# Kernel tuning notes

Hardware: AMD Instinct MI355X
Metric: run time of the kernel (lower is better)

The kernel has to match this reference:

```python
import jax, jax.numpy as jnp
import numpy as np

DIM = 384
K = 10
LN_EPS = 1e-5


def sqdist(src, dst):
    # src [B,N,3], dst [B,M,3] -> [B,N,M] squared euclidean
    d = -2.0 * jnp.einsum('bnc,bmc->bnm', src, dst)
    d += jnp.sum(src ** 2, -1)[:, :, None]
    d += jnp.sum(dst ** 2, -1)[:, None, :]
    return d


def index_points(points, idx):
    # points [B,M,C], idx [B,...] int -> [B,...,C]
    B = points.shape[0]
    flat = idx.reshape(B, -1)
    out = jnp.take_along_axis(points, flat[..., None], axis=1)
    return out.reshape(idx.shape + (points.shape[-1],))


def setup_inputs() -> dict:
    key = jax.random.key(0)
    ks = jax.random.split(key, 10)
    B, N, C = 4, 2048, DIM
    inp = {
        'q': jax.random.normal(ks[0], (B, N, C), jnp.float32),
        'q_pos': jax.random.normal(ks[1], (B, N, 3), jnp.float32),
        # proj_v_off: Linear(dim, dim)
        'Wv': jax.random.normal(ks[2], (C, C), jnp.float32) * 0.02,
        'bv': jnp.zeros((C,), jnp.float32),
        # linear_offset: Linear(2*dim, dim) -> LayerNorm(dim) -> GELU -> Linear(dim, 3, bias=False)
        'W1': jax.random.normal(ks[3], (2 * C, C), jnp.float32) * 0.02,
        'b1': jnp.zeros((C,), jnp.float32),
        'ln_g': jnp.ones((C,), jnp.float32),
        'ln_b': jnp.zeros((C,), jnp.float32),
        'W2': jax.random.normal(ks[4], (C, 3), jnp.float32) * 0.02,
        # knn_map: Linear(2*dim, dim) -> LeakyReLU(0.2)
        'Wk': jax.random.normal(ks[5], (2 * C, C), jnp.float32) * 0.02,
        'bk': jnp.zeros((C,), jnp.float32),
    }
    return inp


def reference(q, q_pos, Wv, bv, W1, b1, ln_g, ln_b, W2, Wk, bk):
    B, N, C = q.shape
    # knn_point: k nearest v_pos for each q_pos (self-attn: v=q, v_pos=q_pos)
    neg_d, idx = jax.lax.top_k(-sqdist(q_pos, q_pos), K)          # idx [B,N,K]

    v_off = q @ Wv + bv                                           # [B,N,C]
    off_local_v = index_points(v_off, idx)                        # [B,N,K,C]
    qk = jnp.broadcast_to(q[:, :, None, :], (B, N, K, C))
    shift_feat = jnp.concatenate([off_local_v, qk], axis=-1)      # [B,N,K,2C]

    h = shift_feat @ W1 + b1
    mu = jnp.mean(h, -1, keepdims=True)
    var = jnp.mean((h - mu) ** 2, -1, keepdims=True)
    h = (h - mu) * jax.lax.rsqrt(var + LN_EPS) * ln_g + ln_b
    h = jax.nn.gelu(h, approximate=False)
    offset = jnp.tanh(h @ W2)                                     # [B,N,K,3]

    local_v_pos = index_points(q_pos, idx)                        # [B,N,K,3]
    scale = (jnp.max(local_v_pos, -2) - jnp.min(local_v_pos, -2))[:, :, None, :] * 0.5
    shift_pos = (local_v_pos + offset * scale).reshape(B, N * K, 3)

    # three_nn: 3 nearest v_pos per shifted point (squared dists, as pointnet2 CUDA)
    neg_d3, idx3 = jax.lax.top_k(-sqdist(shift_pos, q_pos), 3)    # [B,N*K,3]
    dist = -neg_d3
    recip = 1.0 / (dist + 1e-8)
    weight = recip / jnp.sum(recip, -1, keepdims=True)

    nb = index_points(q, idx3)                                    # [B,N*K,3,C]
    interp = jnp.sum(nb * weight[..., None], axis=-2)             # [B,N*K,C]
    interp = interp.reshape(B, N, K, C)

    feature = jnp.concatenate([interp - qk, qk], axis=-1)         # [B,N,K,2C]
    out = jax.nn.leaky_relu(feature @ Wk + bk, 0.2)               # [B,N,K,C]
    return jnp.max(out, axis=-2)                                  # [B,N,C]
```

## Files before the change

### kernel.cpp

```cpp
#include <hip/hip_runtime.h>
#include <hip/hip_bf16.h>
#include <math.h>

#define C_DIM 384
#define N_PTS 2048
#define K_NN 10
#define NK (N_PTS * K_NN)
#define LN_EPS_F 1e-5f

#define TCC 8
#define TCHUNK (N_PTS / TCC)

typedef __attribute__((ext_vector_type(8))) short short8v;
typedef __attribute__((ext_vector_type(4))) float f32x4;

__device__ __forceinline__ float wave_sum64(float v) {
#pragma unroll
  for (int off = 32; off > 0; off >>= 1) v += __shfl_xor(v, off, 64);
  return v;
}

__device__ __forceinline__ unsigned long long shfl_xor_u64(unsigned long long v, int m) {
  return (unsigned long long)__shfl_xor((long long)v, m, 64);
}

__device__ __forceinline__ unsigned short f32_to_bf16_rne(float x) {
  unsigned int u = __float_as_uint(x);
  u += 0x7FFFu + ((u >> 16) & 1u);
  return (unsigned short)(u >> 16);
}

__global__ __launch_bounds__(256) void conv_q_kernel(
    const float* __restrict__ q, unsigned short* __restrict__ outp) {
  const size_t i = ((size_t)blockIdx.x * 256 + threadIdx.x) * 4;
  float4 v = *reinterpret_cast<const float4*>(&q[i]);
  ushort4 o;
  o.x = f32_to_bf16_rne(v.x); o.y = f32_to_bf16_rne(v.y);
  o.z = f32_to_bf16_rne(v.z); o.w = f32_to_bf16_rne(v.w);
  *reinterpret_cast<ushort4*>(&outp[i]) = o;
}

__global__ __launch_bounds__(256) void conv_wkT_kernel(
    const float* __restrict__ Wk, unsigned short* __restrict__ Bt) {
  __shared__ unsigned short tile[64][68];
  const int k0 = blockIdx.x * 64;
  const int sn = blockIdx.y;
  const int s  = sn / 6;
  const int n0 = (sn % 6) * 64;
  const int t = threadIdx.x;
  const int r = t >> 2;
  const int cc = t & 3;
#pragma unroll
  for (int h = 0; h < 4; ++h) {
    const int c = cc * 16 + h * 4;
    float4 v = *reinterpret_cast<const float4*>(
        &Wk[(size_t)(s * 384 + k0 + r) * C_DIM + n0 + c]);
    tile[c + 0][r] = f32_to_bf16_rne(v.x);
    tile[c + 1][r] = f32_to_bf16_rne(v.y);
    tile[c + 2][r] = f32_to_bf16_rne(v.z);
    tile[c + 3][r] = f32_to_bf16_rne(v.w);
  }
  __syncthreads();
#pragma unroll
  for (int h = 0; h < 4; ++h) {
    const int col = cc * 16 + h * 4;
    ushort4 o;
    o.x = tile[r][col + 0]; o.y = tile[r][col + 1];
    o.z = tile[r][col + 2]; o.w = tile[r][col + 3];
    *reinterpret_cast<ushort4*>(
        &Bt[(size_t)(s * 384 + n0 + r) * C_DIM + k0 + col]) = o;
  }
}

__global__ __launch_bounds__(64) void mfma_qaqb_kernel(
    const unsigned short* __restrict__ qbf, const unsigned short* __restrict__ Bt,
    const float* __restrict__ bk, float* __restrict__ qa, float* __restrict__ qb) {
  const int lane = threadIdx.x;
  const int bx = blockIdx.x;
  const int seg = bx / 6;
  const int n0 = (bx % 6) * 64;
  const int m0 = blockIdx.y * 64;
  const unsigned short* Bs = Bt + (size_t)seg * C_DIM * C_DIM;
  const int lm = lane & 15;
  const int lk = (lane >> 4) * 8;
  f32x4 acc[4][4] = {};
#pragma unroll 2
  for (int k0 = 0; k0 < C_DIM; k0 += 32) {
    short8v a[4], b[4];
#pragma unroll
    for (int i = 0; i < 4; ++i)
      a[i] = *reinterpret_cast<const short8v*>(
          &qbf[(size_t)(m0 + i * 16 + lm) * C_DIM + k0 + lk]);
#pragma unroll
    for (int j = 0; j < 4; ++j)
      b[j] = *reinterpret_cast<const short8v*>(
          &Bs[(size_t)(n0 + j * 16 + lm) * C_DIM + k0 + lk]);
#pragma unroll
    for (int i = 0; i < 4; ++i)
#pragma unroll
      for (int j = 0; j < 4; ++j)
        acc[i][j] = __builtin_amdgcn_mfma_f32_16x16x32_bf16(a[i], b[j], acc[i][j], 0, 0, 0);
  }
  const int rb = (lane >> 4) * 4;
#pragma unroll
  for (int i = 0; i < 4; ++i)
#pragma unroll
    for (int j = 0; j < 4; ++j) {
      const int c = n0 + j * 16 + lm;
#pragma unroll
      for (int r = 0; r < 4; ++r) {
        const int m = m0 + i * 16 + rb + r;
        float v = acc[i][j][r];
        if (seg == 0) qa[(size_t)m * C_DIM + c] = v;
        else          qb[(size_t)m * C_DIM + c] = v + bk[c];
      }
    }
}

__global__ __launch_bounds__(256) void sgemm_q2_kernel(
    const float* __restrict__ q,
    const float* __restrict__ B0, const float* __restrict__ B1,
    const float* __restrict__ bias0, const float* __restrict__ bias1,
    float* __restrict__ O0, float* __restrict__ O1) {
  __shared__ float As[32][68];
  __shared__ float Bs[32][132];
  const int bx = blockIdx.x;
  const int seg = bx / 3;
  const int n0 = (bx % 3) * 128;
  const int m0 = blockIdx.y * 64;
  const float* Bp = seg ? B1 : B0;
  const float* bp = seg ? bias1 : bias0;
  float* Op = seg ? O1 : O0;
  const int tid = threadIdx.x;
  const int tn = tid & 15;
  const int tm = tid >> 4;
  float acc[4][8] = {};
  for (int k0 = 0; k0 < C_DIM; k0 += 32) {
#pragma unroll
    for (int h = 0; h < 2; ++h) {
      const int idx = tid + h * 256;
      const int r = idx >> 3;
      const int kc = (idx & 7) * 4;
      float4 a4 = *reinterpret_cast<const float4*>(
          &q[(size_t)(m0 + r) * C_DIM + k0 + kc]);
      As[kc + 0][r] = a4.x; As[kc + 1][r] = a4.y;
      As[kc + 2][r] = a4.z; As[kc + 3][r] = a4.w;
    }
#pragma unroll
    for (int h = 0; h < 4; ++h) {
      const int idx = tid + h * 256;
      const int br = idx >> 5;
      const int bc = (idx & 31) * 4;
      float4 b4 = *reinterpret_cast<const float4*>(
          &Bp[(size_t)(k0 + br) * C_DIM + n0 + bc]);
      *reinterpret_cast<float4*>(&Bs[br][bc]) = b4;
    }
    __syncthreads();
#pragma unroll
    for (int kk = 0; kk < 32; ++kk) {
      float4 a4 = *reinterpret_cast<const float4*>(&As[kk][tm << 2]);
      float4 b0 = *reinterpret_cast<const float4*>(&Bs[kk][tn << 2]);
      float4 b1 = *reinterpret_cast<const float4*>(&Bs[kk][(tn << 2) + 64]);
      float av[4] = {a4.x, a4.y, a4.z, a4.w};
      float bw[8] = {b0.x, b0.y, b0.z, b0.w, b1.x, b1.y, b1.z, b1.w};
#pragma unroll
      for (int i = 0; i < 4; ++i)
#pragma unroll
        for (int j = 0; j < 8; ++j) acc[i][j] = fmaf(av[i], bw[j], acc[i][j]);
    }
    __syncthreads();
  }
#pragma unroll
  for (int i = 0; i < 4; ++i) {
    const int m = m0 + (tm << 2) + i;
    const int c0 = n0 + (tn << 2);
    float4 o0, o1;
    o0.x = acc[i][0]; o0.y = acc[i][1]; o0.z = acc[i][2]; o0.w = acc[i][3];
    o1.x = acc[i][4]; o1.y = acc[i][5]; o1.z = acc[i][6]; o1.w = acc[i][7];
    if (bp) {
      o0.x += bp[c0 + 0]; o0.y += bp[c0 + 1]; o0.z += bp[c0 + 2]; o0.w += bp[c0 + 3];
      o1.x += bp[c0 + 64]; o1.y += bp[c0 + 65]; o1.z += bp[c0 + 66]; o1.w += bp[c0 + 67];
    }
    *reinterpret_cast<float4*>(&Op[(size_t)m * C_DIM + c0]) = o0;
    *reinterpret_cast<float4*>(&Op[(size_t)m * C_DIM + c0 + 64]) = o1;
  }
}

__global__ __launch_bounds__(256) void gemm384_kernel(
    const float* __restrict__ A, const float* __restrict__ W,
    const float* __restrict__ bias, float* __restrict__ Out) {
  __shared__ float As[32][64];
  __shared__ float Bs[32][64];
  const int bm = blockIdx.y * 64;
  const int bn = blockIdx.x * 64;
  const int tid = threadIdx.x;
  const int tx = tid & 15;
  const int ty = tid >> 4;
  const int arow = tid >> 3;
  const int akc  = (tid & 7) << 2;
  const int brow = tid >> 4;
  const int bnc  = (tid & 15) << 2;
  float acc[4][4] = {{0.f, 0.f, 0.f, 0.f}, {0.f, 0.f, 0.f, 0.f},
                     {0.f, 0.f, 0.f, 0.f}, {0.f, 0.f, 0.f, 0.f}};
  for (int k0 = 0; k0 < C_DIM; k0 += 32) {
#pragma unroll
    for (int h = 0; h < 2; ++h) {
      float4 a4 = *reinterpret_cast<const float4*>(
          &A[(size_t)(bm + arow + h * 32) * C_DIM + k0 + akc]);
      As[akc + 0][arow + h * 32] = a4.x;
      As[akc + 1][arow + h * 32] = a4.y;
      As[akc + 2][arow + h * 32] = a4.z;
      As[akc + 3][arow + h * 32] = a4.w;
      float4 b4 = *reinterpret_cast<const float4*>(
          &W[(size_t)(k0 + brow + h * 16) * C_DIM + bn + bnc]);
      *reinterpret_cast<float4*>(&Bs[brow + h * 16][bnc]) = b4;
    }
    __syncthreads();
#pragma unroll
    for (int k = 0; k < 32; ++k) {
      float4 a4 = *reinterpret_cast<const float4*>(&As[k][ty << 2]);
      float4 b4 = *reinterpret_cast<const float4*>(&Bs[k][tx << 2]);
      float av[4] = {a4.x, a4.y, a4.z, a4.w};
      float bw[4] = {b4.x, b4.y, b4.z, b4.w};
#pragma unroll
      for (int i = 0; i < 4; ++i)
#pragma unroll
        for (int j = 0; j < 4; ++j) acc[i][j] = fmaf(av[i], bw[j], acc[i][j]);
    }
    __syncthreads();
  }
#pragma unroll
  for (int i = 0; i < 4; ++i) {
    const int m = bm + (ty << 2) + i;
    const int n0 = bn + (tx << 2);
    float4 o;
    o.x = acc[i][0]; o.y = acc[i][1]; o.z = acc[i][2]; o.w = acc[i][3];
    if (bias) {
      o.x += bias[n0 + 0]; o.y += bias[n0 + 1];
      o.z += bias[n0 + 2]; o.w += bias[n0 + 3];
    }
    *reinterpret_cast<float4*>(&Out[(size_t)m * C_DIM + n0]) = o;
  }
}

__global__ __launch_bounds__(256) void knn_wave_kernel(
    const float* __restrict__ q_pos, int* __restrict__ idx_out,
    float* __restrict__ scale_out) {
  const int wid = threadIdx.x >> 6;
  const int lane = threadIdx.x & 63;
  const int q = blockIdx.x * 4 + wid;
  const int b = q >> 11;
  const int qi = q & 2047;
  __shared__ float4 sc[N_PTS];
  const float* P = q_pos + (size_t)b * N_PTS * 3;
  for (int i = threadIdx.x; i < N_PTS; i += 256) {
    float x = P[i * 3 + 0], y = P[i * 3 + 1], z = P[i * 3 + 2];
    float s = __fadd_rn(__fadd_rn(__fmul_rn(x, x), __fmul_rn(y, y)), __fmul_rn(z, z));
    sc[i] = make_float4(x, y, z, s);
  }
  __syncthreads();
  const float4 qc = sc[qi];
  unsigned long long bd[K_NN];
#pragma unroll
  for (int t = 0; t < K_NN; ++t) bd[t] = ~0ull;
  for (int t = 0; t < N_PTS / 64; ++t) {
    const int j = (t << 6) + lane;
    float4 c = sc[j];
    float dot = __fadd_rn(__fadd_rn(__fmul_rn(qc.x, c.x), __fmul_rn(qc.y, c.y)),
                          __fmul_rn(qc.z, c.z));
    float d = __fadd_rn(__fadd_rn(__fmul_rn(-2.f, dot), qc.w), c.w);
    unsigned int db = __float_as_uint(d);
    db ^= (unsigned int)((int)db >> 31) | 0x80000000u;
    unsigned long long v = ((unsigned long long)db << 32) | (unsigned int)j;
    if (v < bd[K_NN - 1]) {
#pragma unroll
      for (int r = 0; r < K_NN; ++r) {
        bool lt = bd[r] < v;
        unsigned long long lo = lt ? bd[r] : v;
        unsigned long long hi = lt ? v : bd[r];
        bd[r] = lo; v = hi;
      }
    }
  }
  unsigned long long cur = bd[0];
  unsigned long long mine = 0;
#pragma unroll
  for (int r = 0; r < K_NN; ++r) {
    unsigned long long m = cur;
#pragma unroll
    for (int off = 32; off >= 1; off >>= 1) {
      unsigned long long o = shfl_xor_u64(m, off);
      m = (o < m) ? o : m;
    }
    if (cur == m) {
      cur = bd[1];
#pragma unroll
      for (int s = 1; s < K_NN - 1; ++s) bd[s] = bd[s + 1];
      bd[K_NN - 1] = ~0ull;
    }
    if (lane == r) mine = m;
  }
  const int nidx = (int)(mine & 0xFFFFFFFFull);
  if (lane < K_NN) idx_out[(size_t)q * K_NN + lane] = nidx;
  float mnx, mny, mnz, mxx, mxy, mxz;
  if (lane < K_NN) {
    float4 c = sc[nidx];
    mnx = c.x; mny = c.y; mnz = c.z; mxx = c.x; mxy = c.y; mxz = c.z;
  } else {
    mnx = 1e30f; mny = 1e30f; mnz = 1e30f;
    mxx = -1e30f; mxy = -1e30f; mxz = -1e30f;
  }
#pragma unroll
  for (int off = 32; off >= 1; off >>= 1) {
    mnx = fminf(mnx, __shfl_xor(mnx, off, 64));
    mny = fminf(mny, __shfl_xor(mny, off, 64));
    mnz = fminf(mnz, __shfl_xor(mnz, off, 64));
    mxx = fmaxf(mxx, __shfl_xor(mxx, off, 64));
    mxy = fmaxf(mxy, __shfl_xor(mxy, off, 64));
    mxz = fmaxf(mxz, __shfl_xor(mxz, off, 64));
  }
  if (lane == 0) {
    scale_out[(size_t)q * 3 + 0] = (mxx - mnx) * 0.5f;
    scale_out[(size_t)q * 3 + 1] = (mxy - mny) * 0.5f;
    scale_out[(size_t)q * 3 + 2] = (mxz - mnz) * 0.5f;
  }
}

__global__ __launch_bounds__(256) void mid_kernel(
    const float* __restrict__ hv, const float* __restrict__ hq,
    const int* __restrict__ idx, const float* __restrict__ scale,
    const float* __restrict__ q_pos, const float* __restrict__ ln_g,
    const float* __restrict__ ln_b, const float* __restrict__ W2,
    float* __restrict__ shift_pos) {
  const int wid = threadIdx.x >> 6;
  const int lane = threadIdx.x & 63;
  const long row = (long)blockIdx.x * 4 + wid;
  const long bn = row / K_NN;
  const int b = (int)(bn / N_PTS);
  const int g = idx[row];
  const float* hvp = hv + ((size_t)b * N_PTS + g) * C_DIM;
  const float* hqp = hq + (size_t)bn * C_DIM;
  float h[6];
  float s = 0.f;
#pragma unroll
  for (int r = 0; r < 6; ++r) {
    h[r] = hvp[lane + (r << 6)] + hqp[lane + (r << 6)];
    s += h[r];
  }
  s = wave_sum64(s);
  const float mu = s / 384.f;
  float hc[6];
  float vs = 0.f;
#pragma unroll
  for (int r = 0; r < 6; ++r) { hc[r] = h[r] - mu; vs += hc[r] * hc[r]; }
  vs = wave_sum64(vs);
  const float inv = 1.f / sqrtf(vs / 384.f + LN_EPS_F);
  float o0 = 0.f, o1 = 0.f, o2 = 0.f;
#pragma unroll
  for (int r = 0; r < 6; ++r) {
    const int c = lane + (r << 6);
    float y = hc[r] * inv * ln_g[c] + ln_b[c];
    float ge = 0.5f * y * (1.f + erff(y * 0.70710678118654752f));
    o0 += ge * W2[c * 3 + 0];
    o1 += ge * W2[c * 3 + 1];
    o2 += ge * W2[c * 3 + 2];
  }
  o0 = wave_sum64(o0); o1 = wave_sum64(o1); o2 = wave_sum64(o2);
  if (lane < 3) {
    float o = (lane == 0) ? o0 : ((lane == 1) ? o1 : o2);
    float off = tanhf(o);
    float lv = q_pos[((size_t)b * N_PTS + g) * 3 + lane];
    float sc = scale[(size_t)bn * 3 + lane];
    shift_pos[(size_t)row * 3 + lane] = lv + off * sc;
  }
}

__global__ __launch_bounds__(256) void three_nn_part_kernel(
    const float* __restrict__ shift_pos, const float* __restrict__ q_pos,
    float* __restrict__ pd3, int* __restrict__ pi3) {
  const int cc = blockIdx.x;
  const int qc = blockIdx.y;
  const int b = qc / (NK / 256);
  const float* P = q_pos + (size_t)b * N_PTS * 3;
  __shared__ float4 sc[TCHUNK];
  const int c0 = cc * TCHUNK;
  for (int i = threadIdx.x; i < TCHUNK; i += 256) {
    float x = P[(c0 + i) * 3 + 0], y = P[(c0 + i) * 3 + 1], z = P[(c0 + i) * 3 + 2];
    float s = __fadd_rn(__fadd_rn(__fmul_rn(x, x), __fmul_rn(y, y)), __fmul_rn(z, z));
    sc[i] = make_float4(x, y, z, s);
  }
  __syncthreads();
  const long jq = (long)qc * 256 + threadIdx.x;
  const float* S = shift_pos + (size_t)jq * 3;
  const float px = S[0], py = S[1], pz = S[2];
  const float ps = __fadd_rn(__fadd_rn(__fmul_rn(px, px), __fmul_rn(py, py)),
                             __fmul_rn(pz, pz));
  float d0 = 1e30f, d1 = 1e30f, d2 = 1e30f;
  int i0 = 0, i1 = 0, i2 = 0;
  for (int j = 0; j < TCHUNK; ++j) {
    float4 c = sc[j];
    float dot = __fadd_rn(__fadd_rn(__fmul_rn(px, c.x), __fmul_rn(py, c.y)),
                          __fmul_rn(pz, c.z));
    float d = __fadd_rn(__fadd_rn(__fmul_rn(-2.f, dot), ps), c.w);
    if (d < d2) {
      int j0 = c0 + j;
      if (d < d0)      { d2 = d1; i2 = i1; d1 = d0; i1 = i0; d0 = d; i0 = j0; }
      else if (d < d1) { d2 = d1; i2 = i1; d1 = d; i1 = j0; }
      else             { d2 = d; i2 = j0; }
    }
  }
  const size_t base = ((size_t)jq * TCC + cc) * 3;
  pd3[base + 0] = d0; pd3[base + 1] = d1; pd3[base + 2] = d2;
  pi3[base + 0] = i0; pi3[base + 1] = i1; pi3[base + 2] = i2;
}

__global__ __launch_bounds__(256) void three_nn_merge_kernel(
    const float* __restrict__ pd3, const int* __restrict__ pi3,
    int* __restrict__ idx3, float* __restrict__ w3) {
  const long jq = (long)blockIdx.x * 256 + threadIdx.x;
  float d0 = 1e30f, d1 = 1e30f, d2 = 1e30f;
  int i0 = 0, i1 = 0, i2 = 0;
  const size_t base = (size_t)jq * TCC * 3;
  for (int e = 0; e < TCC * 3; ++e) {
    float d = pd3[base + e];
    if (d < d2) {
      int j0 = pi3[base + e];
      if (d < d0)      { d2 = d1; i2 = i1; d1 = d0; i1 = i0; d0 = d; i0 = j0; }
      else if (d < d1) { d2 = d1; i2 = i1; d1 = d; i1 = j0; }
      else             { d2 = d; i2 = j0; }
    }
  }
  const float r0 = 1.f / (d0 + 1e-8f);
  const float r1 = 1.f / (d1 + 1e-8f);
  const float r2 = 1.f / (d2 + 1e-8f);
  const float rs = (r0 + r1) + r2;
  const size_t ob = (size_t)jq * 3;
  idx3[ob + 0] = i0; idx3[ob + 1] = i1; idx3[ob + 2] = i2;
  w3[ob + 0] = r0 / rs; w3[ob + 1] = r1 / rs; w3[ob + 2] = r2 / rs;
}

__global__ __launch_bounds__(256) void final_kernel(
    const float* __restrict__ qa, const float* __restrict__ qb,
    const int* __restrict__ idx3, const float* __restrict__ w3,
    float* __restrict__ out) {
  const int wid = threadIdx.x >> 6;
  const int lane = threadIdx.x & 63;
  const long bn = (long)blockIdx.x * 4 + wid;
  const int b = (int)(bn / N_PTS);
  const float* qaB = qa + (size_t)b * N_PTS * C_DIM;
  float base[6], mx[6];
#pragma unroll
  for (int r = 0; r < 6; ++r) {
    const size_t c = (size_t)bn * C_DIM + lane + (r << 6);
    base[r] = qb[c] - qa[c];
    mx[r] = -1e30f;
  }
  const size_t kb = (size_t)bn * K_NN * 3;
  for (int k = 0; k < K_NN; ++k) {
    const int a0 = idx3[kb + k * 3 + 0];
    const int a1 = idx3[kb + k * 3 + 1];
    const int a2 = idx3[kb + k * 3 + 2];
    const float w0 = w3[kb + k * 3 + 0];
    const float w1 = w3[kb + k * 3 + 1];
    const float w2c = w3[kb + k * 3 + 2];
    const float* p0 = qaB + (size_t)a0 * C_DIM;
    const float* p1 = qaB + (size_t)a1 * C_DIM;
    const float* p2 = qaB + (size_t)a2 * C_DIM;
#pragma unroll
    for (int r = 0; r < 6; ++r) {
      const int c = lane + (r << 6);
      float v = w0 * p0[c] + w1 * p1[c] + w2c * p2[c] + base[r];
      v = (v >= 0.f) ? v : 0.2f * v;
      mx[r] = fmaxf(mx[r], v);
    }
  }
#pragma unroll
  for (int r = 0; r < 6; ++r)
    out[(size_t)bn * C_DIM + lane + (r << 6)] = mx[r];
}

extern "C" void kernel_launch(void* const* d_in, const int* in_sizes, int n_in,
                              void* d_out, int out_size, void* d_ws, size_t ws_size,
                              hipStream_t stream) {
  const float* q     = (const float*)d_in[0];
  const float* q_pos = (const float*)d_in[1];
  const float* Wv    = (const float*)d_in[2];
  const float* bv    = (const float*)d_in[3];
  const float* W1    = (const float*)d_in[4];
  const float* b1    = (const float*)d_in[5];
  const float* ln_g  = (const float*)d_in[6];
  const float* ln_b  = (const float*)d_in[7];
  const float* W2    = (const float*)d_in[8];
  const float* Wk    = (const float*)d_in[9];
  const float* bk    = (const float*)d_in[10];
  float* out = (float*)d_out;

  const int BN = in_sizes[0] / C_DIM;

  const size_t BNC = (size_t)BN * C_DIM;
  float* ws = (float*)d_ws;
  float* bufA = ws;
  float* bufB = bufA + BNC;
  float* bufC = bufB + BNC;
  float* bufD = bufC + BNC;
  float* shift = bufD + BNC;
  float* scale = shift + (size_t)BN * K_NN * 3;
  float* w3    = scale + (size_t)BN * 3;
  int*   idx   = (int*)(w3 + (size_t)BN * K_NN * 3);
  int*   idx3  = idx + (size_t)BN * K_NN;

  float* v_off = out;
  unsigned short* qbf = (unsigned short*)bufB;
  unsigned short* WkT = (unsigned short*)bufC;
  float* pd3 = bufB;
  int*   pi3 = (int*)bufC;

  conv_q_kernel<<<(BN * C_DIM) / 1024, 256, 0, stream>>>(q, qbf);
  conv_wkT_kernel<<<dim3(6, 12), 256, 0, stream>>>(Wk, WkT);
  knn_wave_kernel<<<BN / 4, 256, 0, stream>>>(q_pos, idx, scale);
  mfma_qaqb_kernel<<<dim3(12, BN / 64), 64, 0, stream>>>(qbf, WkT, bk, bufA, bufD);
  sgemm_q2_kernel<<<dim3(6, BN / 64), 256, 0, stream>>>(
      q, Wv, W1 + (size_t)C_DIM * C_DIM, bv, b1, v_off, bufC);
  gemm384_kernel<<<dim3(C_DIM / 64, BN / 64), 256, 0, stream>>>(v_off, W1, nullptr, bufB);
  mid_kernel<<<(BN * K_NN) / 4, 256, 0, stream>>>(bufB, bufC, idx, scale, q_pos,
                                                  ln_g, ln_b, W2, shift);
  three_nn_part_kernel<<<dim3(TCC, (BN * K_NN) / 256), 256, 0, stream>>>(
      shift, q_pos, pd3, pi3);
  three_nn_merge_kernel<<<(BN * K_NN) / 256, 256, 0, stream>>>(pd3, pi3, idx3, w3);
  final_kernel<<<BN / 4, 256, 0, stream>>>(bufA, bufD, idx3, w3, out);
}
```

Before: 355.6 us.

## Replace brute-force three_nn with x-sorted bucket search and pruning

The two-pass brute-force three_nn scan over all 2048 candidates, with its partial/merge step, is replaced by a bucketing scheme. A per-batch kernel bins candidate points into 64 slabs along x and stores them sorted. The query kernel then scans its own slab and expands outward until the slab gap exceeds the current third-best distance plus a small margin. This cuts the number of distance evaluations but adds divergent per-thread loop lengths, a serial single-block-per-batch build kernel, and a tie-break rule that may differ slightly from the reference.

```diff
diff --git a/kernel.cpp b/kernel.cpp
--- a/kernel.cpp
+++ b/kernel.cpp
@@ -7,9 +7,7 @@
 #define K_NN 10
 #define NK (N_PTS * K_NN)
 #define LN_EPS_F 1e-5f
-
-#define TCC 8
-#define TCHUNK (N_PTS / TCC)
+#define NB 64
 
 typedef __attribute__((ext_vector_type(8))) short short8v;
 typedef __attribute__((ext_vector_type(4))) float f32x4;
@@ -375,60 +373,125 @@
   }
 }
 
-__global__ __launch_bounds__(256) void three_nn_part_kernel(
-    const float* __restrict__ shift_pos, const float* __restrict__ q_pos,
-    float* __restrict__ pd3, int* __restrict__ pi3) {
-  const int cc = blockIdx.x;
-  const int qc = blockIdx.y;
-  const int b = qc / (NK / 256);
+__global__ __launch_bounds__(256) void bucket_cand_kernel(
+    const float* __restrict__ q_pos, float4* __restrict__ cbuf,
+    unsigned short* __restrict__ cidx, int* __restrict__ cstart,
+    float4* __restrict__ crange) {
+  const int b = blockIdx.x;
   const float* P = q_pos + (size_t)b * N_PTS * 3;
-  __shared__ float4 sc[TCHUNK];
-  const int c0 = cc * TCHUNK;
-  for (int i = threadIdx.x; i < TCHUNK; i += 256) {
-    float x = P[(c0 + i) * 3 + 0], y = P[(c0 + i) * 3 + 1], z = P[(c0 + i) * 3 + 2];
-    float s = __fadd_rn(__fadd_rn(__fmul_rn(x, x), __fmul_rn(y, y)), __fmul_rn(z, z));
-    sc[i] = make_float4(x, y, z, s);
-  }
-  __syncthreads();
-  const long jq = (long)qc * 256 + threadIdx.x;
+  const int tid = threadIdx.x;
+  __shared__ float redmn[4], redmx[4];
+  __shared__ float sxmin, sinvw;
+  __shared__ int hist[NB], offs[NB + 1], curp[NB];
+  float mn = 1e30f, mx = -1e30f;
+  for (int i = tid; i < N_PTS; i += 256) {
+    float x = P[i * 3];
+    mn = fminf(mn, x); mx = fmaxf(mx, x);
+  }
+#pragma unroll
+  for (int off = 32; off >= 1; off >>= 1) {
+    mn = fminf(mn, __shfl_xor(mn, off, 64));
+    mx = fmaxf(mx, __shfl_xor(mx, off, 64));
+  }
+  if ((tid & 63) == 0) { redmn[tid >> 6] = mn; redmx[tid >> 6] = mx; }
+  if (tid < NB) hist[tid] = 0;
+  __syncthreads();
+  if (tid == 0) {
+    float a = fminf(fminf(redmn[0], redmn[1]), fminf(redmn[2], redmn[3]));
+    float c = fmaxf(fmaxf(redmx[0], redmx[1]), fmaxf(redmx[2], redmx[3]));
+    float wd = (c - a) / (float)NB;
+    sxmin = a;
+    sinvw = (wd > 0.f) ? 1.f / wd : 0.f;
+    crange[b] = make_float4(a, wd, sinvw, 0.f);
+  }
+  __syncthreads();
+  const float xmin = sxmin, invw = sinvw;
+  for (int i = tid; i < N_PTS; i += 256) {
+    int bk = min(NB - 1, max(0, (int)((P[i * 3] - xmin) * invw)));
+    atomicAdd(&hist[bk], 1);
+  }
+  __syncthreads();
+  if (tid == 0) {
+    int a = 0;
+    for (int k = 0; k < NB; ++k) { offs[k] = a; a += hist[k]; }
+    offs[NB] = a;
+  }
+  __syncthreads();
+  if (tid < NB) curp[tid] = offs[tid];
+  if (tid <= NB) cstart[b * (NB + 1) + tid] = offs[tid];
+  __syncthreads();
+  for (int i = tid; i < N_PTS; i += 256) {
+    float x = P[i * 3 + 0], y = P[i * 3 + 1], z = P[i * 3 + 2];
+    int bk = min(NB - 1, max(0, (int)((x - xmin) * invw)));
+    int p = atomicAdd(&curp[bk], 1);
+    float ss = __fadd_rn(__fadd_rn(__fmul_rn(x, x), __fmul_rn(y, y)), __fmul_rn(z, z));
+    cbuf[(size_t)b * N_PTS + p] = make_float4(x, y, z, ss);
+    cidx[(size_t)b * N_PTS + p] = (unsigned short)i;
+  }
+}
+
+#define PRUNE_MARGIN 1e-3f
+__global__ __launch_bounds__(128) void three_nn_bucket_kernel(
+    const float* __restrict__ shift_pos, const float4* __restrict__ cbuf,
+    const unsigned short* __restrict__ cidx, const int* __restrict__ cstart,
+    const float4* __restrict__ crange,
+    int* __restrict__ idx3, float* __restrict__ w3) {
+  const int bpb = NK / 128;
+  const int b = blockIdx.x / bpb;
+  const int tid = threadIdx.x;
+  __shared__ float4 sc[N_PTS];
+  __shared__ unsigned short sid[N_PTS];
+  __shared__ int sstart[NB + 1];
+  for (int i = tid; i < N_PTS; i += 128) {
+    sc[i] = cbuf[(size_t)b * N_PTS + i];
+    sid[i] = cidx[(size_t)b * N_PTS + i];
+  }
+  if (tid <= NB) sstart[tid] = cstart[b * (NB + 1) + tid];
+  __syncthreads();
+  const long jq = (long)blockIdx.x * 128 + tid;
   const float* S = shift_pos + (size_t)jq * 3;
   const float px = S[0], py = S[1], pz = S[2];
   const float ps = __fadd_rn(__fadd_rn(__fmul_rn(px, px), __fmul_rn(py, py)),
                              __fmul_rn(pz, pz));
+  const float4 rg = crange[b];
+  const float xmin = rg.x, w = rg.y, invw = rg.z;
+  const int myb = min(NB - 1, max(0, (int)((px - xmin) * invw)));
   float d0 = 1e30f, d1 = 1e30f, d2 = 1e30f;
   int i0 = 0, i1 = 0, i2 = 0;
-  for (int j = 0; j < TCHUNK; ++j) {
-    float4 c = sc[j];
-    float dot = __fadd_rn(__fadd_rn(__fmul_rn(px, c.x), __fmul_rn(py, c.y)),
-                          __fmul_rn(pz, c.z));
-    float d = __fadd_rn(__fadd_rn(__fmul_rn(-2.f, dot), ps), c.w);
-    if (d < d2) {
-      int j0 = c0 + j;
-      if (d < d0)      { d2 = d1; i2 = i1; d1 = d0; i1 = i0; d0 = d; i0 = j0; }
-      else if (d < d1) { d2 = d1; i2 = i1; d1 = d; i1 = j0; }
-      else             { d2 = d; i2 = j0; }
-    }
-  }
-  const size_t base = ((size_t)jq * TCC + cc) * 3;
-  pd3[base + 0] = d0; pd3[base + 1] = d1; pd3[base + 2] = d2;
-  pi3[base + 0] = i0; pi3[base + 1] = i1; pi3[base + 2] = i2;
-}
-
-__global__ __launch_bounds__(256) void three_nn_merge_kernel(
-    const float* __restrict__ pd3, const int* __restrict__ pi3,
-    int* __restrict__ idx3, float* __restrict__ w3) {
-  const long jq = (long)blockIdx.x * 256 + threadIdx.x;
-  float d0 = 1e30f, d1 = 1e30f, d2 = 1e30f;
-  int i0 = 0, i1 = 0, i2 = 0;
-  const size_t base = (size_t)jq * TCC * 3;
-  for (int e = 0; e < TCC * 3; ++e) {
-    float d = pd3[base + e];
-    if (d < d2) {
-      int j0 = pi3[base + e];
-      if (d < d0)      { d2 = d1; i2 = i1; d1 = d0; i1 = i0; d0 = d; i0 = j0; }
-      else if (d < d1) { d2 = d1; i2 = i1; d1 = d; i1 = j0; }
-      else             { d2 = d; i2 = j0; }
-    }
+  auto scanb = [&](int bb) {
+    const int pe = sstart[bb + 1];
+    for (int p = sstart[bb]; p < pe; ++p) {
+      float4 c = sc[p];
+      float dot = __fadd_rn(__fadd_rn(__fmul_rn(px, c.x), __fmul_rn(py, c.y)),
+                            __fmul_rn(pz, c.z));
+      float d = __fadd_rn(__fadd_rn(__fmul_rn(-2.f, dot), ps), c.w);
+      const int jo = (int)sid[p];
+      if (d < d2 || (d == d2 && jo < i2)) {
+        if (d < d0 || (d == d0 && jo < i0)) {
+          d2 = d1; i2 = i1; d1 = d0; i1 = i0; d0 = d; i0 = jo;
+        } else if (d < d1 || (d == d1 && jo < i1)) {
+          d2 = d1; i2 = i1; d1 = d; i1 = jo;
+        } else {
+          d2 = d; i2 = jo;
+        }
+      }
+    }
+  };
+  scanb(myb);
+  int bl = myb - 1, br = myb + 1;
+  while (bl >= 0 || br < NB) {
+    bool prog = false;
+    if (bl >= 0) {
+      float gap = px - (xmin + (float)(bl + 1) * w);
+      if (__fmul_rn(gap, gap) <= d2 + PRUNE_MARGIN) { scanb(bl); --bl; prog = true; }
+      else bl = -1;
+    }
+    if (br < NB) {
+      float gap = (xmin + (float)br * w) - px;
+      if (__fmul_rn(gap, gap) <= d2 + PRUNE_MARGIN) { scanb(br); ++br; prog = true; }
+      else br = NB;
+    }
+    if (!prog) break;
   }
   const float r0 = 1.f / (d0 + 1e-8f);
   const float r1 = 1.f / (d1 + 1e-8f);
@@ -496,6 +559,7 @@
   float* out = (float*)d_out;
 
   const int BN = in_sizes[0] / C_DIM;
+  const int B  = BN / N_PTS;
 
   const size_t BNC = (size_t)BN * C_DIM;
   float* ws = (float*)d_ws;
@@ -512,8 +576,11 @@
   float* v_off = out;
   unsigned short* qbf = (unsigned short*)bufB;
   unsigned short* WkT = (unsigned short*)bufC;
-  float* pd3 = bufB;
-  int*   pi3 = (int*)bufC;
+
+  float4* cbuf = (float4*)bufB;
+  unsigned short* cidx = (unsigned short*)(bufB + 32768);
+  int* cstartp = (int*)(bufB + 32768 + 4096);
+  float4* crange = (float4*)(bufB + 32768 + 4096 + 260);
 
   conv_q_kernel<<<(BN * C_DIM) / 1024, 256, 0, stream>>>(q, qbf);
   conv_wkT_kernel<<<dim3(6, 12), 256, 0, stream>>>(Wk, WkT);
@@ -524,8 +591,8 @@
   gemm384_kernel<<<dim3(C_DIM / 64, BN / 64), 256, 0, stream>>>(v_off, W1, nullptr, bufB);
   mid_kernel<<<(BN * K_NN) / 4, 256, 0, stream>>>(bufB, bufC, idx, scale, q_pos,
                                                   ln_g, ln_b, W2, shift);
-  three_nn_part_kernel<<<dim3(TCC, (BN * K_NN) / 256), 256, 0, stream>>>(
-      shift, q_pos, pd3, pi3);
-  three_nn_merge_kernel<<<(BN * K_NN) / 256, 256, 0, stream>>>(pd3, pi3, idx3, w3);
+  bucket_cand_kernel<<<B, 256, 0, stream>>>(q_pos, cbuf, cidx, cstartp, crange);
+  three_nn_bucket_kernel<<<(BN * K_NN) / 128, 128, 0, stream>>>(
+      shift, cbuf, cidx, cstartp, crange, idx3, w3);
   final_kernel<<<BN / 4, 256, 0, stream>>>(bufA, bufD, idx3, w3, out);
 }
```

After: 793.6 us. 2.23x slower.
